# Performance work log

Measured on AMD Instinct MI355X. Metric: run time of the kernel, lower is better.

The kernel has to match this reference:

```python
import jax, jax.numpy as jnp
import numpy as np

MARGIN = 0.2


def setup_inputs() -> dict:
    key = jax.random.key(0)
    k1, k2 = jax.random.split(key)
    N, D, C = 512, 256, 64
    embeddings = jax.random.normal(k1, (N, D), dtype=jnp.float32)
    labels = jax.random.randint(k2, (N,), 0, C, dtype=jnp.int64)
    return {"embeddings": embeddings, "labels": labels}


def reference(embeddings, labels):
    # Faithful vectorization of the python-loop semi-hard triplet mining.
    # The original iterates unordered positive pairs (i<j) and treats BOTH i and j
    # as anchors, i.e. all ordered positive pairs (a, p), a != p, labels[a]==labels[p].
    # For each such pair it picks a uniformly-random negative n with
    #   pd[a,n] > pd[a,p]  and  pd[a,n]^2 < pd[a,p]^2 + margin,
    # and the loss only uses SQUARED distances, so we work with sqd directly
    # (all comparisons are monotone in the square for non-negative distances).
    n = embeddings.shape[0]
    sq_norm = jnp.sum(embeddings * embeddings, axis=-1)  # [N]
    # squared pairwise distances (== torch.cdist(...)**2), clamped for fp error
    sqd = jnp.maximum(sq_norm[:, None] + sq_norm[None, :]
                      - 2.0 * (embeddings @ embeddings.T), 0.0)  # [N, N]

    same = labels[:, None] == labels[None, :]                     # [N, N]
    pos_pair = same & ~jnp.eye(n, dtype=bool)                     # ordered positive pairs (a, p)

    # valid[a, p, j]: j is an admissible negative for anchor a w.r.t. positive p
    d_ap = sqd[:, :, None]        # sqd[a, p] broadcast over j
    d_aj = sqd[:, None, :]        # sqd[a, j] broadcast over p
    valid = (~same)[:, None, :] & (d_aj > d_ap) & (d_aj < d_ap + MARGIN)  # [N, N, N]
    has_neg = jnp.any(valid, axis=-1)                             # [N, N]

    # uniform random choice among valid negatives via Gumbel-argmax
    gumbel = jax.random.gumbel(jax.random.key(42), (n, n, n), dtype=jnp.float32)
    scores = jnp.where(valid, gumbel, -jnp.inf)
    j_star = jnp.argmax(scores, axis=-1)                          # [N, N]
    d_an_sq = jnp.take_along_axis(sqd, j_star, axis=1)            # sqd[a, j_star[a, p]]

    contrib = (pos_pair & has_neg).astype(sqd.dtype)              # [N, N]
    terms = sqd - d_an_sq + MARGIN                                # d_ap^2 - d_an^2 + margin
    count = jnp.maximum(jnp.sum(contrib), 1.0)
    loss = jnp.sum(terms * contrib) / count
    return loss
```

## Files before the change

### kernel.cpp

```cpp
#include <hip/hip_runtime.h>
#include <cstdint>

#define NPTS 512
#define DIM 256
#define NBLK (NPTS / 2)
#define MARGIN_F 0.2f
#define FIX_SCALE 1099511627776.0

__device__ __forceinline__ uint32_t rotl32(uint32_t x, uint32_t r) {
  return (x << r) | (x >> (32u - r));
}

__device__ __forceinline__ uint32_t threefry_bits(uint32_t c1) {
  const uint32_t k0 = 0u, k1 = 42u;
  const uint32_t k2 = k0 ^ k1 ^ 0x1BD11BDAu;
  uint32_t x0 = 0u + k0;
  uint32_t x1 = c1 + k1;
#define TFR(r) { x0 += x1; x1 = rotl32(x1, r); x1 ^= x0; }
  TFR(13u) TFR(15u) TFR(26u) TFR(6u)
  x0 += k1; x1 += k2 + 1u;
  TFR(17u) TFR(29u) TFR(16u) TFR(24u)
  x0 += k2; x1 += k0 + 2u;
  TFR(13u) TFR(15u) TFR(26u) TFR(6u)
  x0 += k0; x1 += k1 + 3u;
  TFR(17u) TFR(29u) TFR(16u) TFR(24u)
  x0 += k1; x1 += k2 + 4u;
  TFR(13u) TFR(15u) TFR(26u) TFR(6u)
  x0 += k2; x1 += k0 + 5u;
#undef TFR
  return x0 ^ x1;
}

__global__ __launch_bounds__(512) void triplet_main(
    const float* __restrict__ emb,
    const int* __restrict__ labels,
    unsigned long long* __restrict__ part)
{
  __shared__ float sea0[DIM];
  __shared__ float sea1[DIM];
  __shared__ float sd0[NPTS];
  __shared__ float sd1[NPTS];
  __shared__ float snrm[NPTS];
  __shared__ int   slab[NPTS];
  __shared__ int   plist[128];
  __shared__ int   pcnt;
  __shared__ unsigned long long wsum[8], wcnt[8];

  const int a0 = blockIdx.x * 2;
  const int a1 = a0 + 1;
  const int t = threadIdx.x;
  const int wave = t >> 6;
  const int lane = t & 63;
  const int grp = lane >> 4;
  const int l16 = lane & 15;

  if (t < 256)       sea0[t]       = emb[a0 * DIM + t];
  else               sea1[t - 256] = emb[a1 * DIM + (t - 256)];
  slab[t] = labels[t];
  if (t == 0) pcnt = 0;
  __syncthreads();

  #pragma unroll 2
  for (int round = 0; round < 16; ++round) {
    const int j = (wave << 6) + (round << 2) + grp;
    float s0 = 0.f, s1 = 0.f, q = 0.f;
    #pragma unroll
    for (int it = 0; it < 4; ++it) {
      const int d = (it << 6) + (l16 << 2);
      const float4 v  = *reinterpret_cast<const float4*>(emb + j * DIM + d);
      const float4 w0 = *reinterpret_cast<const float4*>(sea0 + d);
      const float4 w1 = *reinterpret_cast<const float4*>(sea1 + d);
      s0 += v.x * w0.x + v.y * w0.y + v.z * w0.z + v.w * w0.w;
      s1 += v.x * w1.x + v.y * w1.y + v.z * w1.z + v.w * w1.w;
      q  += v.x * v.x  + v.y * v.y  + v.z * v.z  + v.w * v.w;
    }
    #pragma unroll
    for (int m = 8; m; m >>= 1) {
      s0 += __shfl_xor(s0, m);
      s1 += __shfl_xor(s1, m);
      q  += __shfl_xor(q, m);
    }
    if (l16 == 0) { sd0[j] = s0; sd1[j] = s1; snrm[j] = q; }
  }
  __syncthreads();

  {
    const float na0 = snrm[a0];
    const float na1 = snrm[a1];
    const float nj = snrm[t];
    const float v0 = na0 + nj - 2.f * sd0[t];
    const float v1 = na1 + nj - 2.f * sd1[t];
    __syncthreads();
    sd0[t] = v0 > 0.f ? v0 : 0.f;
    sd1[t] = v1 > 0.f ? v1 : 0.f;
    const int lp = slab[t];
    if (t != a0 && lp == slab[a0]) { int k = atomicAdd(&pcnt, 1); plist[k] = t; }
    if (t != a1 && lp == slab[a1]) { int k = atomicAdd(&pcnt, 1); plist[k] = (1 << 16) | t; }
  }
  __syncthreads();

  unsigned long long lsum = 0ull, lcnt = 0ull;
  const int np = pcnt;
  for (int e = wave; e < np; e += 8) {
    const int ent = plist[e];
    const int ai = ent >> 16;
    const int p = ent & 0xffff;
    const float* drp = ai ? sd1 : sd0;
    const int ag = ai ? a1 : a0;
    const int la = slab[ag];
    const float dap = drp[p];
    const float hi = dap + MARGIN_F;
    const uint32_t base = ((uint32_t)ag << 18) | ((uint32_t)p << 9);

    int bestKey = -1, bestJ = 0;
    #pragma unroll
    for (int k = 0; k < 8; ++k) {
      const int j = lane + (k << 6);
      const float dj = drp[j];
      if (slab[j] != la && dj > dap && dj < hi) {
        const int key = (int)(threefry_bits(base + (uint32_t)j) >> 9);
        if (key > bestKey) { bestKey = key; bestJ = j; }
      }
    }
    #pragma unroll
    for (int m = 32; m; m >>= 1) {
      const int ok = __shfl_xor(bestKey, m);
      const int oj = __shfl_xor(bestJ, m);
      if (ok > bestKey || (ok == bestKey && oj < bestJ)) { bestKey = ok; bestJ = oj; }
    }
    if (lane == 0 && bestKey >= 0) {
      const float term = (dap - drp[bestJ]) + MARGIN_F;
      lsum += (unsigned long long)((double)term * FIX_SCALE + 0.5);
      lcnt += 1ull;
    }
  }

  if (lane == 0) { wsum[wave] = lsum; wcnt[wave] = lcnt; }
  __syncthreads();
  if (t == 0) {
    unsigned long long s = 0ull, c = 0ull;
    #pragma unroll
    for (int w = 0; w < 8; ++w) { s += wsum[w]; c += wcnt[w]; }
    part[2 * blockIdx.x]     = s;
    part[2 * blockIdx.x + 1] = c;
  }
}

__global__ __launch_bounds__(64) void triplet_finalize(
    const unsigned long long* __restrict__ part,
    float* __restrict__ out)
{
  const int lane = threadIdx.x;
  unsigned long long s = 0ull, c = 0ull;
  #pragma unroll
  for (int k = 0; k < NBLK / 64; ++k) {
    const int b = lane + (k << 6);
    s += part[2 * b];
    c += part[2 * b + 1];
  }
  #pragma unroll
  for (int m = 32; m; m >>= 1) {
    s += __shfl_xor(s, m);
    c += __shfl_xor(c, m);
  }
  if (lane == 0) {
    const double sd = (double)s / FIX_SCALE;
    const double cd = c ? (double)c : 1.0;
    out[0] = (float)(sd / cd);
  }
}

extern "C" void kernel_launch(void* const* d_in, const int* in_sizes, int n_in,
                              void* d_out, int out_size, void* d_ws, size_t ws_size,
                              hipStream_t stream) {
  const float* emb  = (const float*)d_in[0];
  const int* labels = (const int*)d_in[1];
  float* out        = (float*)d_out;
  unsigned long long* part = (unsigned long long*)d_ws;

  triplet_main<<<dim3(NBLK), dim3(512), 0, stream>>>(emb, labels, part);
  triplet_finalize<<<dim3(1), dim3(64), 0, stream>>>(part, out);
}
```

Baseline: 20.48 us.

## Fuse finalize into main kernel via packed atomic accumulator and hoist anchor loads

Drops the separate finalize kernel. Each block atomically adds one packed 64-bit word holding a done-counter, a pair count and a fixed-point sum, and the last block to arrive writes the final mean. The two anchor rows are also hoisted from shared memory into registers, and the row loads are issued before the dot products with deeper unrolling. A memset launch takes the place of the finalize launch. The fixed-point scale drops to 2^30 with limited bit fields, which lowers precision and risks overflow of the sum or count fields.

Result: slower. 24.28 us (+18.5%).

```diff
diff --git a/kernel.cpp b/kernel.cpp
--- a/kernel.cpp
+++ b/kernel.cpp
@@ -5,7 +5,10 @@
 #define DIM 256
 #define NBLK (NPTS / 2)
 #define MARGIN_F 0.2f
-#define FIX_SCALE 1099511627776.0
+#define FIX_SCALE 1073741824.0
+#define SUM_BITS 42
+#define CNT_SHIFT 42
+#define DONE_SHIFT 56
 
 __device__ __forceinline__ uint32_t rotl32(uint32_t x, uint32_t r) {
   return (x << r) | (x >> (32u - r));
@@ -34,7 +37,8 @@
 __global__ __launch_bounds__(512) void triplet_main(
     const float* __restrict__ emb,
     const int* __restrict__ labels,
-    unsigned long long* __restrict__ part)
+    unsigned long long* __restrict__ acc,
+    float* __restrict__ out)
 {
   __shared__ float sea0[DIM];
   __shared__ float sea1[DIM];
@@ -60,19 +64,28 @@
   if (t == 0) pcnt = 0;
   __syncthreads();
 
-  #pragma unroll 2
+  float4 A0[4], A1[4];
+  #pragma unroll
+  for (int it = 0; it < 4; ++it) {
+    const int d = (it << 6) + (l16 << 2);
+    A0[it] = *reinterpret_cast<const float4*>(sea0 + d);
+    A1[it] = *reinterpret_cast<const float4*>(sea1 + d);
+  }
+
+  #pragma unroll 4
   for (int round = 0; round < 16; ++round) {
     const int j = (wave << 6) + (round << 2) + grp;
+    const float4* rj = reinterpret_cast<const float4*>(emb + j * DIM);
+    float4 v[4];
+    #pragma unroll
+    for (int it = 0; it < 4; ++it) v[it] = rj[(it << 4) + l16];
+
     float s0 = 0.f, s1 = 0.f, q = 0.f;
     #pragma unroll
     for (int it = 0; it < 4; ++it) {
-      const int d = (it << 6) + (l16 << 2);
-      const float4 v  = *reinterpret_cast<const float4*>(emb + j * DIM + d);
-      const float4 w0 = *reinterpret_cast<const float4*>(sea0 + d);
-      const float4 w1 = *reinterpret_cast<const float4*>(sea1 + d);
-      s0 += v.x * w0.x + v.y * w0.y + v.z * w0.z + v.w * w0.w;
-      s1 += v.x * w1.x + v.y * w1.y + v.z * w1.z + v.w * w1.w;
-      q  += v.x * v.x  + v.y * v.y  + v.z * v.z  + v.w * v.w;
+      s0 += v[it].x * A0[it].x + v[it].y * A0[it].y + v[it].z * A0[it].z + v[it].w * A0[it].w;
+      s1 += v[it].x * A1[it].x + v[it].y * A1[it].y + v[it].z * A1[it].z + v[it].w * A1[it].w;
+      q  += v[it].x * v[it].x  + v[it].y * v[it].y  + v[it].z * v[it].z  + v[it].w * v[it].w;
     }
     #pragma unroll
     for (int m = 8; m; m >>= 1) {
@@ -141,32 +154,17 @@
     unsigned long long s = 0ull, c = 0ull;
     #pragma unroll
     for (int w = 0; w < 8; ++w) { s += wsum[w]; c += wcnt[w]; }
-    part[2 * blockIdx.x]     = s;
-    part[2 * blockIdx.x + 1] = c;
-  }
-}
-
-__global__ __launch_bounds__(64) void triplet_finalize(
-    const unsigned long long* __restrict__ part,
-    float* __restrict__ out)
-{
-  const int lane = threadIdx.x;
-  unsigned long long s = 0ull, c = 0ull;
-  #pragma unroll
-  for (int k = 0; k < NBLK / 64; ++k) {
-    const int b = lane + (k << 6);
-    s += part[2 * b];
-    c += part[2 * b + 1];
-  }
-  #pragma unroll
-  for (int m = 32; m; m >>= 1) {
-    s += __shfl_xor(s, m);
-    c += __shfl_xor(c, m);
-  }
-  if (lane == 0) {
-    const double sd = (double)s / FIX_SCALE;
-    const double cd = c ? (double)c : 1.0;
-    out[0] = (float)(sd / cd);
+    const unsigned long long contrib =
+        (1ull << DONE_SHIFT) | (c << CNT_SHIFT) | s;
+    const unsigned long long old = atomicAdd(acc, contrib);
+    if ((old >> DONE_SHIFT) == (unsigned long long)(NBLK - 1)) {
+      const unsigned long long tot = old + contrib;
+      const unsigned long long sum = tot & ((1ull << SUM_BITS) - 1ull);
+      const unsigned long long cnt = (tot >> CNT_SHIFT) & 0x3FFFull;
+      const double sd = (double)sum / FIX_SCALE;
+      const double cd = cnt ? (double)cnt : 1.0;
+      out[0] = (float)(sd / cd);
+    }
   }
 }
 
@@ -176,8 +174,8 @@
   const float* emb  = (const float*)d_in[0];
   const int* labels = (const int*)d_in[1];
   float* out        = (float*)d_out;
-  unsigned long long* part = (unsigned long long*)d_ws;
+  unsigned long long* acc = (unsigned long long*)d_ws;
 
-  triplet_main<<<dim3(NBLK), dim3(512), 0, stream>>>(emb, labels, part);
-  triplet_finalize<<<dim3(1), dim3(64), 0, stream>>>(part, out);
+  hipMemsetAsync(d_ws, 0, sizeof(unsigned long long), stream);
+  triplet_main<<<dim3(NBLK), dim3(512), 0, stream>>>(emb, labels, acc, out);
 }
```
